# Performance work log

Hardware: AMD Instinct MI355X
Metric: run time of the kernel (lower is better)

The kernel has to match this reference:

```python
import jax, jax.numpy as jnp
import numpy as np

N, E, D, H, ED, L = 50000, 800000, 256, 8, 16, 6
C = D // H  # 32
NEG_SLOPE = 0.2
EPS = 1e-5


def setup_inputs() -> dict:
    key = jax.random.key(0)
    ks = jax.random.split(key, 16)
    f32 = jnp.float32
    return {
        "x": jax.random.normal(ks[0], (N, D), f32),
        "edge_index": jax.random.randint(ks[1], (2, E), 0, N, dtype=jnp.int64),
        "edge_attr": jax.random.normal(ks[2], (E, ED), f32),
        # shared GATConv params (single conv reused every step, as in the source)
        "W": jax.random.normal(ks[3], (D, D), f32) / np.sqrt(D),
        "att_src": jax.random.normal(ks[4], (H, C), f32) * 0.05,
        "att_dst": jax.random.normal(ks[5], (H, C), f32) * 0.05,
        "att_edge": jax.random.normal(ks[6], (H, C), f32) * 0.05,
        "W_edge": jax.random.normal(ks[7], (ED, D), f32) / np.sqrt(ED),
        "bias": jnp.zeros((D,), f32),
        # per-step FFN + LayerNorm params
        "ffn_w1": jax.random.normal(ks[8], (L, D, 4 * D), f32) / np.sqrt(D),
        "ffn_b1": jnp.zeros((L, 4 * D), f32),
        "ffn_w2": jax.random.normal(ks[9], (L, 4 * D, D), f32) / np.sqrt(4 * D),
        "ffn_b2": jnp.zeros((L, D), f32),
        "ln1_g": jnp.ones((L, D), f32),
        "ln1_b": jnp.zeros((L, D), f32),
        "ln2_g": jnp.ones((L, D), f32),
        "ln2_b": jnp.zeros((L, D), f32),
    }


def _layernorm(x, g, b):
    mu = jnp.mean(x, -1, keepdims=True)
    var = jnp.mean(jnp.square(x - mu), -1, keepdims=True)
    return (x - mu) * jax.lax.rsqrt(var + EPS) * g + b


def _gat_conv(m, edge_index, edge_attr, W, att_src, att_dst, att_edge, W_edge, bias):
    n = m.shape[0]
    x_proj = (m @ W).reshape(n, H, C)  # [N,H,C]
    # add self loops; edge_attr fill_value='mean' (PyG default): mean of incoming edge feats
    src0, dst0 = edge_index[0], edge_index[1]
    deg = jax.ops.segment_sum(jnp.ones_like(dst0, jnp.float32), dst0, n)
    ea_mean = jax.ops.segment_sum(edge_attr, dst0, n) / jnp.maximum(deg, 1.0)[:, None]
    loop = jnp.arange(n, dtype=src0.dtype)
    src = jnp.concatenate([src0, loop])
    dst = jnp.concatenate([dst0, loop])
    ea = jnp.concatenate([edge_attr, ea_mean], 0)
    e_proj = (ea @ W_edge).reshape(-1, H, C)  # [E+N,H,C]
    a_src = jnp.sum(x_proj * att_src, -1)  # [N,H]
    a_dst = jnp.sum(x_proj * att_dst, -1)  # [N,H]
    a_edge = jnp.sum(e_proj * att_edge, -1)  # [E+N,H]
    alpha = jax.nn.leaky_relu(a_src[src] + a_dst[dst] + a_edge, NEG_SLOPE)
    # softmax over edges grouped by destination node
    amax = jax.ops.segment_max(alpha, dst, n)  # every node has a self loop
    ex = jnp.exp(alpha - amax[dst])
    denom = jax.ops.segment_sum(ex, dst, n)
    attn = ex / denom[dst]  # [E+N,H]
    msg = x_proj[src] * attn[:, :, None]  # [E+N,H,C]
    out = jax.ops.segment_sum(msg, dst, n).reshape(n, H * C)
    return out + bias


def reference(x, edge_index, edge_attr, W, att_src, att_dst, att_edge, W_edge, bias,
              ffn_w1, ffn_b1, ffn_w2, ffn_b2, ln1_g, ln1_b, ln2_g, ln2_b):
    m = x
    for i in range(L):
        g = _gat_conv(m, edge_index, edge_attr, W, att_src, att_dst, att_edge, W_edge, bias)
        m = _layernorm(g + m, ln1_g[i], ln1_b[i])  # dropout is identity in eval
        h = jax.nn.relu(m @ ffn_w1[i] + ffn_b1[i]) @ ffn_w2[i] + ffn_b2[i]
        m = _layernorm(h + m, ln2_g[i], ln2_b[i])
    return m
```

## Files before the change

kernel.cpp:

```cpp
#include <hip/hip_runtime.h>
#include <math.h>

#define NN 50000
#define MP 50048
#define EE 800000
#define DD 256
#define HH 8
#define CC 32
#define EDIMK 16
#define LL 6
#define HID 1024
#define NEG 0.2f
#define LNEPS 1e-5f
#define NPARTS ((NN + 255) / 256)

using short8   = __attribute__((ext_vector_type(8))) short;
using ushort8  = __attribute__((ext_vector_type(8))) unsigned short;
using floatx4  = __attribute__((ext_vector_type(4))) float;

static __device__ __forceinline__ float4 ld4(const float* p) {
    return *reinterpret_cast<const float4*>(p);
}
static __device__ __forceinline__ void st4(float* p, float4 v) {
    *reinterpret_cast<float4*>(p) = v;
}
static __device__ __forceinline__ float b2f(unsigned short u) {
    union { unsigned int i; float f; } v; v.i = ((unsigned int)u) << 16; return v.f;
}
static __device__ __forceinline__ unsigned short f2b(float f) {
    union { float f; unsigned int i; } v; v.f = f;
    unsigned int r = (v.i + 0x7fffu + ((v.i >> 16) & 1u)) >> 16;
    return (unsigned short)r;
}
static __device__ __forceinline__ void gload_lds16(const ushort* g, ushort* l) {
    __builtin_amdgcn_global_load_lds((const __attribute__((address_space(1))) void*)g,
                                     (__attribute__((address_space(3))) void*)l, 16, 0, 0);
}

__global__ void k_weh(const float* __restrict__ W_edge, const float* __restrict__ att_edge,
                      float* __restrict__ w_eh) {
    int t = threadIdx.x;
    if (t < EDIMK * HH) {
        int k = t >> 3, h = t & 7;
        float s = 0.f;
        for (int c = 0; c < CC; ++c) s += W_edge[k * DD + h * CC + c] * att_edge[h * CC + c];
        w_eh[t] = s;
    }
}

__global__ void k_edge_pre(const float* __restrict__ edge_attr, const int* __restrict__ ei,
                           const float* __restrict__ w_eh, float* __restrict__ a_edge,
                           int* __restrict__ deg) {
    __shared__ float sw[EDIMK * HH];
    if (threadIdx.x < EDIMK * HH) sw[threadIdx.x] = w_eh[threadIdx.x];
    __syncthreads();
    int e = blockIdx.x * blockDim.x + threadIdx.x;
    if (e >= EE) return;
    float ea[EDIMK];
#pragma unroll
    for (int k4 = 0; k4 < EDIMK; k4 += 4) {
        float4 v = ld4(edge_attr + (size_t)e * EDIMK + k4);
        ea[k4] = v.x; ea[k4 + 1] = v.y; ea[k4 + 2] = v.z; ea[k4 + 3] = v.w;
    }
#pragma unroll
    for (int h = 0; h < HH; ++h) {
        float s = 0.f;
#pragma unroll
        for (int k = 0; k < EDIMK; ++k) s += ea[k] * sw[k * HH + h];
        a_edge[(size_t)e * HH + h] = s;
    }
    atomicAdd(&deg[ei[EE + e]], 1);
}

__global__ __launch_bounds__(256) void k_scan1(const int* __restrict__ deg,
                                               int* __restrict__ rowptr,
                                               int* __restrict__ part) {
    __shared__ int wsum[4];
    int tid = threadIdx.x, wid = tid >> 6, lane = tid & 63;
    int g = blockIdx.x * 256 + tid;
    int v = (g < NN) ? deg[g] : 0;
    int s = v;
#pragma unroll
    for (int off = 1; off < 64; off <<= 1) {
        int t = __shfl_up(s, off, 64);
        if (lane >= off) s += t;
    }
    if (lane == 63) wsum[wid] = s;
    __syncthreads();
    int woff = 0;
    for (int i = 0; i < wid; ++i) woff += wsum[i];
    s += woff;
    if (g < NN) rowptr[g + 1] = s;
    if (tid == 255) part[blockIdx.x] = s;
}
__global__ __launch_bounds__(256) void k_scan2(int* __restrict__ part) {
    __shared__ int wsum[4];
    int tid = threadIdx.x, wid = tid >> 6, lane = tid & 63;
    int v = (tid < NPARTS) ? part[tid] : 0;
    int s = v;
#pragma unroll
    for (int off = 1; off < 64; off <<= 1) {
        int t = __shfl_up(s, off, 64);
        if (lane >= off) s += t;
    }
    if (lane == 63) wsum[wid] = s;
    __syncthreads();
    int woff = 0;
    for (int i = 0; i < wid; ++i) woff += wsum[i];
    s += woff;
    if (tid < NPARTS) part[tid] = s - v;
}
__global__ __launch_bounds__(256) void k_scan3(int* __restrict__ rowptr,
                                               const int* __restrict__ part) {
    int g = blockIdx.x * 256 + threadIdx.x;
    if (g == 0) rowptr[0] = 0;
    if (g < NN) rowptr[g + 1] += part[blockIdx.x];
}

__global__ void k_scatter(const int* __restrict__ ei, const int* __restrict__ rowptr,
                          int* __restrict__ cursor, int* __restrict__ s_src,
                          int* __restrict__ s_eid) {
    int e = blockIdx.x * blockDim.x + threadIdx.x;
    if (e >= EE) return;
    int dst = ei[EE + e];
    int p = rowptr[dst] + atomicAdd(&cursor[dst], 1);
    s_src[p] = ei[e];
    s_eid[p] = e;
}

__global__ void k_permute(const int* __restrict__ s_eid, const float* __restrict__ a_edge,
                          float* __restrict__ ae_csr) {
    size_t t = (size_t)blockIdx.x * blockDim.x + threadIdx.x;
    if (t >= (size_t)EE * HH) return;
    ae_csr[t] = a_edge[(size_t)s_eid[t >> 3] * HH + (t & 7)];
}

__global__ void k_selfmean(const int* __restrict__ rowptr, const float* __restrict__ ae_csr,
                           float* __restrict__ a_self) {
    int t = blockIdx.x * blockDim.x + threadIdx.x;
    if (t >= NN * HH) return;
    int n = t >> 3, h = t & 7;
    int k0 = rowptr[n], k1 = rowptr[n + 1];
    float s = 0.f;
    for (int k = k0; k < k1; ++k) s += ae_csr[(size_t)k * HH + h];
    int d = k1 - k0; if (d < 1) d = 1;
    a_self[t] = s / (float)d;
}

__global__ __launch_bounds__(1024) void k_trans(const float* __restrict__ src,
                                                ushort* __restrict__ dst, int K, int N) {
    __shared__ float s[32][33];
    const float* S = src + (size_t)blockIdx.z * K * N;
    ushort* D = dst + (size_t)blockIdx.z * K * N;
    int n0 = blockIdx.x * 32, k0 = blockIdx.y * 32;
    s[threadIdx.y][threadIdx.x] = S[(size_t)(k0 + threadIdx.y) * N + n0 + threadIdx.x];
    __syncthreads();
    D[(size_t)(n0 + threadIdx.y) * K + k0 + threadIdx.x] = f2b(s[threadIdx.x][threadIdx.y]);
}

__global__ void k_cvt(const float* __restrict__ x, float* __restrict__ m,
                      ushort* __restrict__ mb) {
    int t = blockIdx.x * blockDim.x + threadIdx.x;
    if (t >= NN * DD) return;
    float v = x[t];
    m[t] = v;
    mb[t] = f2b(v);
}

__global__ __launch_bounds__(256) void k_gemm_bf16(const ushort* __restrict__ A,
                                                   const ushort* __restrict__ Bt,
                                                   const float* __restrict__ bias,
                                                   void* __restrict__ Cout,
                                                   int Nc, int K, int mode) {
    __shared__ ushort As[128 * 64];
    __shared__ ushort Bs[128 * 64];
    int tid = threadIdx.x;
    int w = tid >> 6, lane = tid & 63;
    int tileM = blockIdx.y * 128, tileN = blockIdx.x * 128;
    const ushort* gA[4]; const ushort* gB[4];
    ushort* lA[4]; ushort* lB[4];
#pragma unroll
    for (int p = 0; p < 4; ++p) {
        int c = (p * 4 + w) * 64 + lane;
        int row = c >> 3, slot = c & 7;
        int gs = slot ^ (row & 7);
        gA[p] = A + (size_t)(tileM + row) * K + gs * 8;
        gB[p] = Bt + (size_t)(tileN + row) * K + gs * 8;
        lA[p] = As + (size_t)c * 8;
        lB[p] = Bs + (size_t)c * 8;
    }
    int wr = w >> 1, wc = w & 1;
    int fr = lane & 15, q = lane >> 4;
    floatx4 acc[4][4] = {};
    for (int k0 = 0; k0 < K; k0 += 64) {
        __syncthreads();
#pragma unroll
        for (int p = 0; p < 4; ++p) gload_lds16(gA[p] + k0, lA[p]);
#pragma unroll
        for (int p = 0; p < 4; ++p) gload_lds16(gB[p] + k0, lB[p]);
        __syncthreads();
#pragma unroll
        for (int kc = 0; kc < 2; ++kc) {
            int ps = ((kc * 4 + q) ^ (fr & 7)) * 8;
            short8 af[4], bf[4];
#pragma unroll
            for (int i = 0; i < 4; ++i)
                af[i] = *(const short8*)(As + (wr * 64 + i * 16 + fr) * 64 + ps);
#pragma unroll
            for (int j = 0; j < 4; ++j)
                bf[j] = *(const short8*)(Bs + (wc * 64 + j * 16 + fr) * 64 + ps);
#pragma unroll
            for (int i = 0; i < 4; ++i)
#pragma unroll
                for (int j = 0; j < 4; ++j)
                    acc[i][j] = __builtin_amdgcn_mfma_f32_16x16x32_bf16(af[i], bf[j], acc[i][j], 0, 0, 0);
        }
    }
    int rbase = tileM + wr * 64 + q * 4;
    int cbase = tileN + wc * 64 + fr;
#pragma unroll
    for (int j = 0; j < 4; ++j) {
        int col = cbase + j * 16;
        float bb = (mode != 1) ? bias[col] : 0.f;
#pragma unroll
        for (int i = 0; i < 4; ++i) {
            int row = rbase + i * 16;
#pragma unroll
            for (int r = 0; r < 4; ++r) {
                float v = acc[i][j][r] + bb;
                if (mode == 2 && v < 0.f) v = 0.f;
                if (mode == 0)
                    ((float*)Cout)[(size_t)(row + r) * Nc + col] = v;
                else
                    ((ushort*)Cout)[(size_t)(row + r) * Nc + col] = f2b(v);
            }
        }
    }
}

__global__ void k_srcdst(const ushort* __restrict__ xb, const float* __restrict__ att_src,
                         const float* __restrict__ att_dst, float* __restrict__ a_src,
                         float* __restrict__ a_dst) {
    __shared__ float ss[DD], sd[DD];
    int tid = threadIdx.x;
    if (tid < DD) { ss[tid] = att_src[tid]; sd[tid] = att_dst[tid]; }
    __syncthreads();
    int t = blockIdx.x * blockDim.x + tid;
    if (t >= NN * HH) return;
    int n = t >> 3, h = t & 7;
    const ushort* xp = xb + (size_t)n * DD + h * CC;
    float s1 = 0.f, s2 = 0.f;
#pragma unroll
    for (int c = 0; c < CC; c += 4) {
        ushort4 u = *(const ushort4*)(xp + c);
        float vx = b2f(u.x), vy = b2f(u.y), vz = b2f(u.z), vw = b2f(u.w);
        int b = h * CC + c;
        s1 += vx * ss[b] + vy * ss[b + 1] + vz * ss[b + 2] + vw * ss[b + 3];
        s2 += vx * sd[b] + vy * sd[b + 1] + vz * sd[b + 2] + vw * sd[b + 3];
    }
    a_src[t] = s1;
    a_dst[t] = s2;
}

__global__ __launch_bounds__(256) void k_agg(const ushort* __restrict__ xb,
                                             const float* __restrict__ a_src,
                                             const float* __restrict__ a_dst,
                                             const float* __restrict__ a_self,
                                             const int* __restrict__ rowptr,
                                             const int* __restrict__ s_src,
                                             const float* __restrict__ ae_csr,
                                             const float* __restrict__ bias,
                                             const float* __restrict__ gma,
                                             const float* __restrict__ bta,
                                             float* __restrict__ m,
                                             ushort* __restrict__ mb) {
    int wid = (blockIdx.x * blockDim.x + threadIdx.x) >> 6;
    int lane = threadIdx.x & 63;
    int n = wid * 2 + (lane >> 5);
    if (n >= NN) return;
    int hl = lane & 31, h = hl >> 2, c8 = hl * 8;
    float adn = a_dst[n * HH + h];
    float al0 = a_src[n * HH + h] + adn + a_self[n * HH + h];
    al0 = al0 > 0.f ? al0 : NEG * al0;
    float w0 = __expf(al0);
    ushort8 xs = *(const ushort8*)(xb + (size_t)n * DD + c8);
    float acc[8];
#pragma unroll
    for (int i = 0; i < 8; ++i) acc[i] = w0 * b2f(xs[i]);
    float den = w0;
    int k = rowptr[n], k1 = rowptr[n + 1];
    for (; k + 1 < k1; k += 2) {
        int s0 = s_src[k], s1 = s_src[k + 1];
        float t0 = a_src[(size_t)s0 * HH + h] + adn + ae_csr[(size_t)k * HH + h];
        float t1 = a_src[(size_t)s1 * HH + h] + adn + ae_csr[(size_t)(k + 1) * HH + h];
        t0 = t0 > 0.f ? t0 : NEG * t0;
        t1 = t1 > 0.f ? t1 : NEG * t1;
        float wv0 = __expf(t0), wv1 = __expf(t1);
        ushort8 v0 = *(const ushort8*)(xb + (size_t)s0 * DD + c8);
        ushort8 v1 = *(const ushort8*)(xb + (size_t)s1 * DD + c8);
        den += wv0 + wv1;
#pragma unroll
        for (int i = 0; i < 8; ++i) acc[i] += wv0 * b2f(v0[i]) + wv1 * b2f(v1[i]);
    }
    if (k < k1) {
        int s0 = s_src[k];
        float t0 = a_src[(size_t)s0 * HH + h] + adn + ae_csr[(size_t)k * HH + h];
        t0 = t0 > 0.f ? t0 : NEG * t0;
        float wv0 = __expf(t0);
        ushort8 v0 = *(const ushort8*)(xb + (size_t)s0 * DD + c8);
        den += wv0;
#pragma unroll
        for (int i = 0; i < 8; ++i) acc[i] += wv0 * b2f(v0[i]);
    }
    float inv = 1.f / den;
    size_t base = (size_t)n * DD + c8;
    float4 mr0 = ld4(m + base), mr1 = ld4(m + base + 4);
    float4 b0 = ld4(bias + c8), b1 = ld4(bias + c8 + 4);
    float g[8];
    g[0] = acc[0] * inv + b0.x + mr0.x; g[1] = acc[1] * inv + b0.y + mr0.y;
    g[2] = acc[2] * inv + b0.z + mr0.z; g[3] = acc[3] * inv + b0.w + mr0.w;
    g[4] = acc[4] * inv + b1.x + mr1.x; g[5] = acc[5] * inv + b1.y + mr1.y;
    g[6] = acc[6] * inv + b1.z + mr1.z; g[7] = acc[7] * inv + b1.w + mr1.w;
    float s = 0.f;
#pragma unroll
    for (int i = 0; i < 8; ++i) s += g[i];
#pragma unroll
    for (int off = 16; off; off >>= 1) s += __shfl_xor(s, off, 64);
    float mu = s * (1.0f / DD);
    float qv = 0.f;
#pragma unroll
    for (int i = 0; i < 8; ++i) { g[i] -= mu; qv += g[i] * g[i]; }
#pragma unroll
    for (int off = 16; off; off >>= 1) qv += __shfl_xor(qv, off, 64);
    float rs = rsqrtf(qv * (1.0f / DD) + LNEPS);
    float4 g0 = ld4(gma + c8), g1 = ld4(gma + c8 + 4);
    float4 bb0 = ld4(bta + c8), bb1 = ld4(bta + c8 + 4);
    float o[8];
    o[0] = g[0] * rs * g0.x + bb0.x; o[1] = g[1] * rs * g0.y + bb0.y;
    o[2] = g[2] * rs * g0.z + bb0.z; o[3] = g[3] * rs * g0.w + bb0.w;
    o[4] = g[4] * rs * g1.x + bb1.x; o[5] = g[5] * rs * g1.y + bb1.y;
    o[6] = g[6] * rs * g1.z + bb1.z; o[7] = g[7] * rs * g1.w + bb1.w;
    st4(m + base, make_float4(o[0], o[1], o[2], o[3]));
    st4(m + base + 4, make_float4(o[4], o[5], o[6], o[7]));
    ushort8 ob;
#pragma unroll
    for (int i = 0; i < 8; ++i) ob[i] = f2b(o[i]);
    *reinterpret_cast<ushort8*>(mb + base) = ob;
}

__global__ __launch_bounds__(256) void k_addln2(const ushort* __restrict__ a,
                                                const float* __restrict__ gma,
                                                const float* __restrict__ bta,
                                                float* __restrict__ m,
                                                ushort* __restrict__ mb) {
    int wid = (blockIdx.x * blockDim.x + threadIdx.x) >> 6;
    int lane = threadIdx.x & 63;
    if (wid >= NN) return;
    size_t base = (size_t)wid * DD + lane * 4;
    ushort4 ua = *(const ushort4*)(a + base);
    float4 vb = ld4(m + base);
    float4 v;
    v.x = b2f(ua.x) + vb.x; v.y = b2f(ua.y) + vb.y;
    v.z = b2f(ua.z) + vb.z; v.w = b2f(ua.w) + vb.w;
    float s = v.x + v.y + v.z + v.w;
    for (int off = 32; off; off >>= 1) s += __shfl_xor(s, off, 64);
    float mu = s * (1.0f / DD);
    float4 d;
    d.x = v.x - mu; d.y = v.y - mu; d.z = v.z - mu; d.w = v.w - mu;
    float qv = d.x * d.x + d.y * d.y + d.z * d.z + d.w * d.w;
    for (int off = 32; off; off >>= 1) qv += __shfl_xor(qv, off, 64);
    float rs = rsqrtf(qv * (1.0f / DD) + LNEPS);
    float4 g4 = ld4(gma + lane * 4), b4 = ld4(bta + lane * 4);
    float4 o;
    o.x = d.x * rs * g4.x + b4.x; o.y = d.y * rs * g4.y + b4.y;
    o.z = d.z * rs * g4.z + b4.z; o.w = d.w * rs * g4.w + b4.w;
    st4(m + base, o);
    ushort4 ob;
    ob.x = f2b(o.x); ob.y = f2b(o.y); ob.z = f2b(o.z); ob.w = f2b(o.w);
    *reinterpret_cast<ushort4*>(mb + base) = ob;
}

extern "C" void kernel_launch(void* const* d_in, const int* in_sizes, int n_in,
                              void* d_out, int out_size, void* d_ws, size_t ws_size,
                              hipStream_t stream) {
    const float* x        = (const float*)d_in[0];
    const int*   ei       = (const int*)d_in[1];
    const float* edge_attr= (const float*)d_in[2];
    const float* W        = (const float*)d_in[3];
    const float* att_src  = (const float*)d_in[4];
    const float* att_dst  = (const float*)d_in[5];
    const float* att_edge = (const float*)d_in[6];
    const float* W_edge   = (const float*)d_in[7];
    const float* bias     = (const float*)d_in[8];
    const float* ffn_w1   = (const float*)d_in[9];
    const float* ffn_b1   = (const float*)d_in[10];
    const float* ffn_w2   = (const float*)d_in[11];
    const float* ffn_b2   = (const float*)d_in[12];
    const float* ln1_g    = (const float*)d_in[13];
    const float* ln1_b    = (const float*)d_in[14];
    const float* ln2_g    = (const float*)d_in[15];
    const float* ln2_b    = (const float*)d_in[16];
    float* m = (float*)d_out;

    char* wp = (char*)d_ws;
    auto alloc = [&](size_t bytes) -> char* {
        char* p = wp;
        wp += (bytes + 255) & ~(size_t)255;
        return p;
    };
    float*  a_edge = (float*)alloc((size_t)EE * HH * 4);
    float*  ae_csr = (float*)alloc((size_t)EE * HH * 4);
    float*  a_self = (float*)alloc((size_t)NN * HH * 4);
    float*  a_src  = (float*)alloc((size_t)NN * HH * 4);
    float*  a_dst  = (float*)alloc((size_t)NN * HH * 4);
    int*    deg    = (int*)alloc((size_t)NN * 4);
    int*    rowptr = (int*)alloc((size_t)(NN + 1) * 4);
    int*    cursor = (int*)alloc((size_t)NN * 4);
    int*    part   = (int*)alloc((size_t)NPARTS * 4);
    int*    s_src  = (int*)alloc((size_t)EE * 4);
    int*    s_eid  = (int*)alloc((size_t)EE * 4);
    float*  w_eh   = (float*)alloc((size_t)EDIMK * HH * 4);
    ushort* Wt     = (ushort*)alloc((size_t)DD * DD * 2);
    ushort* w1t    = (ushort*)alloc((size_t)LL * DD * HID * 2);
    ushort* w2t    = (ushort*)alloc((size_t)LL * HID * DD * 2);
    ushort* xprojb = (ushort*)alloc((size_t)MP * DD * 2);
    ushort* m_b    = (ushort*)alloc((size_t)MP * DD * 2);
    ushort* gbuf   = (ushort*)alloc((size_t)MP * DD * 2);
    size_t used = (size_t)(wp - (char*)d_ws);
    size_t avail = ws_size > used ? ws_size - used : 0;
    size_t maxrows = avail / ((size_t)HID * 2);
    int chunkP = (int)((maxrows / 128) * 128);
    if (chunkP < 128) chunkP = 128;
    if (chunkP > MP) chunkP = MP;
    ushort* h1b = (ushort*)wp;

    hipMemsetAsync(deg, 0, (size_t)NN * 4, stream);
    hipMemsetAsync(cursor, 0, (size_t)NN * 4, stream);

    k_weh<<<1, 128, 0, stream>>>(W_edge, att_edge, w_eh);
    k_edge_pre<<<(EE + 255) / 256, 256, 0, stream>>>(edge_attr, ei, w_eh, a_edge, deg);
    k_scan1<<<NPARTS, 256, 0, stream>>>(deg, rowptr, part);
    k_scan2<<<1, 256, 0, stream>>>(part);
    k_scan3<<<NPARTS, 256, 0, stream>>>(rowptr, part);
    k_scatter<<<(EE + 255) / 256, 256, 0, stream>>>(ei, rowptr, cursor, s_src, s_eid);
    k_permute<<<(EE * HH + 255) / 256, 256, 0, stream>>>(s_eid, a_edge, ae_csr);
    k_selfmean<<<(NN * HH + 255) / 256, 256, 0, stream>>>(rowptr, ae_csr, a_self);
    k_trans<<<dim3(DD / 32, DD / 32, 1), dim3(32, 32), 0, stream>>>(W, Wt, DD, DD);
    k_trans<<<dim3(HID / 32, DD / 32, LL), dim3(32, 32), 0, stream>>>(ffn_w1, w1t, DD, HID);
    k_trans<<<dim3(DD / 32, HID / 32, LL), dim3(32, 32), 0, stream>>>(ffn_w2, w2t, HID, DD);
    k_cvt<<<(NN * DD + 255) / 256, 256, 0, stream>>>(x, m, m_b);

    for (int i = 0; i < LL; ++i) {
        k_gemm_bf16<<<dim3(DD / 128, MP / 128), 256, 0, stream>>>(m_b, Wt, nullptr, xprojb, DD, DD, 1);
        k_srcdst<<<(NN * HH + 255) / 256, 256, 0, stream>>>(xprojb, att_src, att_dst, a_src, a_dst);
        k_agg<<<((NN + 1) / 2 * 64 + 255) / 256, 256, 0, stream>>>(xprojb, a_src, a_dst, a_self,
                                                                   rowptr, s_src, ae_csr, bias,
                                                                   ln1_g + i * DD, ln1_b + i * DD, m, m_b);
        for (int r0 = 0; r0 < MP; r0 += chunkP) {
            int rows = (MP - r0) < chunkP ? (MP - r0) : chunkP;
            k_gemm_bf16<<<dim3(HID / 128, rows / 128), 256, 0, stream>>>(
                m_b + (size_t)r0 * DD, w1t + (size_t)i * DD * HID,
                ffn_b1 + (size_t)i * HID, h1b, HID, DD, 2);
            k_gemm_bf16<<<dim3(DD / 128, rows / 128), 256, 0, stream>>>(
                h1b, w2t + (size_t)i * HID * DD,
                ffn_b2 + (size_t)i * DD, gbuf + (size_t)r0 * DD, DD, HID, 3);
        }
        k_addln2<<<(NN * 64 + 255) / 256, 256, 0, stream>>>(gbuf, ln2_g + i * DD, ln2_b + i * DD, m, m_b);
    }
}
```

Baseline: 2.000 ms.

## Fuse FFN second GEMM with residual add and LayerNorm; unroll aggregation by four

Adds a dedicated GEMM kernel whose 64-row tile spans the full 256 output columns. This lets it add bias and residual and compute LayerNorm in the epilogue, with a cross-wave reduction through shared memory. The separate add+LN kernel and the bf16 intermediate buffer go away, along with their global memory round trip. The GAT aggregation loop is also unrolled from two to four edges so more gathers are in flight at once. The tradeoffs are a smaller M tile with 40KB of shared memory, which may lower occupancy and B reuse, and a variance computed as E[x^2]-mu^2, which is less numerically stable.

```diff
diff --git a/kernel.cpp b/kernel.cpp
--- a/kernel.cpp
+++ b/kernel.cpp
@@ -229,10 +229,111 @@
             for (int r = 0; r < 4; ++r) {
                 float v = acc[i][j][r] + bb;
                 if (mode == 2 && v < 0.f) v = 0.f;
-                if (mode == 0)
-                    ((float*)Cout)[(size_t)(row + r) * Nc + col] = v;
-                else
-                    ((ushort*)Cout)[(size_t)(row + r) * Nc + col] = f2b(v);
+                ((ushort*)Cout)[(size_t)(row + r) * Nc + col] = f2b(v);
+            }
+        }
+    }
+}
+
+__global__ __launch_bounds__(256) void k_gemm2_ln(const ushort* __restrict__ A,
+                                                  const ushort* __restrict__ Bt,
+                                                  const float* __restrict__ bias,
+                                                  const float* __restrict__ gma,
+                                                  const float* __restrict__ bta,
+                                                  float* __restrict__ m,
+                                                  ushort* __restrict__ mb,
+                                                  int rowsValid) {
+    __shared__ ushort As[64 * 64];
+    __shared__ ushort Bs[256 * 64];
+    __shared__ float redS[64][4];
+    __shared__ float redQ[64][4];
+    const int K = HID;
+    int tid = threadIdx.x;
+    int w = tid >> 6, lane = tid & 63;
+    int tileM = blockIdx.x * 64;
+    int rA = tid >> 3, sl = tid & 7;
+    int gs = sl ^ (rA & 7);
+    const ushort* gA = A + (size_t)(tileM + rA) * K + gs * 8;
+    const ushort* gB = Bt + (size_t)rA * K + gs * 8;
+    ushort* lA = As + (size_t)tid * 8;
+    ushort* lB = Bs + (size_t)tid * 8;
+    int fr = lane & 15, q = lane >> 4;
+    floatx4 acc[4][4] = {};
+    for (int k0 = 0; k0 < K; k0 += 64) {
+        __syncthreads();
+        gload_lds16(gA + k0, lA);
+        gload_lds16(gA + (size_t)32 * K + k0, lA + 256 * 8);
+#pragma unroll
+        for (int p = 0; p < 8; ++p)
+            gload_lds16(gB + (size_t)p * 32 * K + k0, lB + (size_t)p * 256 * 8);
+        __syncthreads();
+#pragma unroll
+        for (int kc = 0; kc < 2; ++kc) {
+            int ps = ((kc * 4 + q) ^ (fr & 7)) * 8;
+            short8 af[4], bf[4];
+#pragma unroll
+            for (int i = 0; i < 4; ++i)
+                af[i] = *(const short8*)(As + (i * 16 + fr) * 64 + ps);
+#pragma unroll
+            for (int j = 0; j < 4; ++j)
+                bf[j] = *(const short8*)(Bs + (w * 64 + j * 16 + fr) * 64 + ps);
+#pragma unroll
+            for (int i = 0; i < 4; ++i)
+#pragma unroll
+                for (int j = 0; j < 4; ++j)
+                    acc[i][j] = __builtin_amdgcn_mfma_f32_16x16x32_bf16(af[i], bf[j], acc[i][j], 0, 0, 0);
+        }
+    }
+    int colb = w * 64 + fr;
+    float bw[4], gw[4], btw[4];
+#pragma unroll
+    for (int j = 0; j < 4; ++j) {
+        bw[j] = bias[colb + j * 16];
+        gw[j] = gma[colb + j * 16];
+        btw[j] = bta[colb + j * 16];
+    }
+#pragma unroll
+    for (int i = 0; i < 4; ++i) {
+#pragma unroll
+        for (int rr = 0; rr < 4; ++rr) {
+            int lrow = i * 16 + q * 4 + rr;
+            int grow = tileM + lrow;
+            bool valid = grow < rowsValid;
+            float s = 0.f, s2 = 0.f;
+#pragma unroll
+            for (int j = 0; j < 4; ++j) {
+                float rres = valid ? m[(size_t)grow * DD + colb + j * 16] : 0.f;
+                float gv = acc[i][j][rr] + bw[j] + rres;
+                acc[i][j][rr] = gv;
+                s += gv; s2 += gv * gv;
+            }
+#pragma unroll
+            for (int msk = 1; msk < 16; msk <<= 1) {
+                s += __shfl_xor(s, msk, 16);
+                s2 += __shfl_xor(s2, msk, 16);
+            }
+            if (fr == 0) { redS[lrow][w] = s; redQ[lrow][w] = s2; }
+        }
+    }
+    __syncthreads();
+#pragma unroll
+    for (int i = 0; i < 4; ++i) {
+#pragma unroll
+        for (int rr = 0; rr < 4; ++rr) {
+            int lrow = i * 16 + q * 4 + rr;
+            int grow = tileM + lrow;
+            if (grow >= rowsValid) continue;
+            float su = redS[lrow][0] + redS[lrow][1] + redS[lrow][2] + redS[lrow][3];
+            float sq = redQ[lrow][0] + redQ[lrow][1] + redQ[lrow][2] + redQ[lrow][3];
+            float mu = su * (1.0f / DD);
+            float var = sq * (1.0f / DD) - mu * mu;
+            float rs = rsqrtf(var + LNEPS);
+#pragma unroll
+            for (int j = 0; j < 4; ++j) {
+                float v = (acc[i][j][rr] - mu) * rs * gw[j] + btw[j];
+                size_t idx = (size_t)grow * DD + colb + j * 16;
+                m[idx] = v;
+                mb[idx] = f2b(v);
             }
         }
     }
@@ -289,20 +390,31 @@
     for (int i = 0; i < 8; ++i) acc[i] = w0 * b2f(xs[i]);
     float den = w0;
     int k = rowptr[n], k1 = rowptr[n + 1];
-    for (; k + 1 < k1; k += 2) {
-        int s0 = s_src[k], s1 = s_src[k + 1];
-        float t0 = a_src[(size_t)s0 * HH + h] + adn + ae_csr[(size_t)k * HH + h];
-        float t1 = a_src[(size_t)s1 * HH + h] + adn + ae_csr[(size_t)(k + 1) * HH + h];
+    for (; k + 3 < k1; k += 4) {
+        int s0 = s_src[k], s1 = s_src[k + 1], s2 = s_src[k + 2], s3 = s_src[k + 3];
+        float e0 = ae_csr[(size_t)k * HH + h];
+        float e1 = ae_csr[(size_t)(k + 1) * HH + h];
+        float e2 = ae_csr[(size_t)(k + 2) * HH + h];
+        float e3 = ae_csr[(size_t)(k + 3) * HH + h];
+        float t0 = a_src[(size_t)s0 * HH + h] + adn + e0;
+        float t1 = a_src[(size_t)s1 * HH + h] + adn + e1;
+        float t2 = a_src[(size_t)s2 * HH + h] + adn + e2;
+        float t3 = a_src[(size_t)s3 * HH + h] + adn + e3;
+        ushort8 v0 = *(const ushort8*)(xb + (size_t)s0 * DD + c8);
+        ushort8 v1 = *(const ushort8*)(xb + (size_t)s1 * DD + c8);
+        ushort8 v2 = *(const ushort8*)(xb + (size_t)s2 * DD + c8);
+        ushort8 v3 = *(const ushort8*)(xb + (size_t)s3 * DD + c8);
         t0 = t0 > 0.f ? t0 : NEG * t0;
         t1 = t1 > 0.f ? t1 : NEG * t1;
-        float wv0 = __expf(t0), wv1 = __expf(t1);
-        ushort8 v0 = *(const ushort8*)(xb + (size_t)s0 * DD + c8);
-        ushort8 v1 = *(const ushort8*)(xb + (size_t)s1 * DD + c8);
-        den += wv0 + wv1;
-#pragma unroll
-        for (int i = 0; i < 8; ++i) acc[i] += wv0 * b2f(v0[i]) + wv1 * b2f(v1[i]);
-    }
-    if (k < k1) {
+        t2 = t2 > 0.f ? t2 : NEG * t2;
+        t3 = t3 > 0.f ? t3 : NEG * t3;
+        float wv0 = __expf(t0), wv1 = __expf(t1), wv2 = __expf(t2), wv3 = __expf(t3);
+        den += (wv0 + wv1) + (wv2 + wv3);
+#pragma unroll
+        for (int i = 0; i < 8; ++i)
+            acc[i] += (wv0 * b2f(v0[i]) + wv1 * b2f(v1[i])) + (wv2 * b2f(v2[i]) + wv3 * b2f(v3[i]));
+    }
+    for (; k < k1; ++k) {
         int s0 = s_src[k];
         float t0 = a_src[(size_t)s0 * HH + h] + adn + ae_csr[(size_t)k * HH + h];
         t0 = t0 > 0.f ? t0 : NEG * t0;
@@ -346,38 +458,6 @@
 #pragma unroll
     for (int i = 0; i < 8; ++i) ob[i] = f2b(o[i]);
     *reinterpret_cast<ushort8*>(mb + base) = ob;
-}
-
-__global__ __launch_bounds__(256) void k_addln2(const ushort* __restrict__ a,
-                                                const float* __restrict__ gma,
-                                                const float* __restrict__ bta,
-                                                float* __restrict__ m,
-                                                ushort* __restrict__ mb) {
-    int wid = (blockIdx.x * blockDim.x + threadIdx.x) >> 6;
-    int lane = threadIdx.x & 63;
-    if (wid >= NN) return;
-    size_t base = (size_t)wid * DD + lane * 4;
-    ushort4 ua = *(const ushort4*)(a + base);
-    float4 vb = ld4(m + base);
-    float4 v;
-    v.x = b2f(ua.x) + vb.x; v.y = b2f(ua.y) + vb.y;
-    v.z = b2f(ua.z) + vb.z; v.w = b2f(ua.w) + vb.w;
-    float s = v.x + v.y + v.z + v.w;
-    for (int off = 32; off; off >>= 1) s += __shfl_xor(s, off, 64);
-    float mu = s * (1.0f / DD);
-    float4 d;
-    d.x = v.x - mu; d.y = v.y - mu; d.z = v.z - mu; d.w = v.w - mu;
-    float qv = d.x * d.x + d.y * d.y + d.z * d.z + d.w * d.w;
-    for (int off = 32; off; off >>= 1) qv += __shfl_xor(qv, off, 64);
-    float rs = rsqrtf(qv * (1.0f / DD) + LNEPS);
-    float4 g4 = ld4(gma + lane * 4), b4 = ld4(bta + lane * 4);
-    float4 o;
-    o.x = d.x * rs * g4.x + b4.x; o.y = d.y * rs * g4.y + b4.y;
-    o.z = d.z * rs * g4.z + b4.z; o.w = d.w * rs * g4.w + b4.w;
-    st4(m + base, o);
-    ushort4 ob;
-    ob.x = f2b(o.x); ob.y = f2b(o.y); ob.z = f2b(o.z); ob.w = f2b(o.w);
-    *reinterpret_cast<ushort4*>(mb + base) = ob;
 }
 
 extern "C" void kernel_launch(void* const* d_in, const int* in_sizes, int n_in,
@@ -425,7 +505,6 @@
     ushort* w2t    = (ushort*)alloc((size_t)LL * HID * DD * 2);
     ushort* xprojb = (ushort*)alloc((size_t)MP * DD * 2);
     ushort* m_b    = (ushort*)alloc((size_t)MP * DD * 2);
-    ushort* gbuf   = (ushort*)alloc((size_t)MP * DD * 2);
     size_t used = (size_t)(wp - (char*)d_ws);
     size_t avail = ws_size > used ? ws_size - used : 0;
     size_t maxrows = avail / ((size_t)HID * 2);
@@ -461,10 +540,10 @@
             k_gemm_bf16<<<dim3(HID / 128, rows / 128), 256, 0, stream>>>(
                 m_b + (size_t)r0 * DD, w1t + (size_t)i * DD * HID,
                 ffn_b1 + (size_t)i * HID, h1b, HID, DD, 2);
-            k_gemm_bf16<<<dim3(DD / 128, rows / 128), 256, 0, stream>>>(
-                h1b, w2t + (size_t)i * HID * DD,
-                ffn_b2 + (size_t)i * DD, gbuf + (size_t)r0 * DD, DD, HID, 3);
+            k_gemm2_ln<<<rows / 64, 256, 0, stream>>>(
+                h1b, w2t + (size_t)i * HID * DD, ffn_b2 + (size_t)i * DD,
+                ln2_g + i * DD, ln2_b + i * DD,
+                m + (size_t)r0 * DD, m_b + (size_t)r0 * DD, NN - r0);
         }
-        k_addln2<<<(NN * 64 + 255) / 256, 256, 0, stream>>>(gbuf, ln2_g + i * DD, ln2_b + i * DD, m, m_b);
-    }
-}
+    }
+}
```

Result: faster. 1.857 ms (-7.1%).
